# Performance work log

Measured on AMD Instinct MI355X. Metric: run time of the kernel, lower is better.

The kernel has to match this reference:

```python
import jax, jax.numpy as jnp
import numpy as np

N, L, S, C, H = 8, 1024, 1024, 256, 8
D = C // H  # 32

def setup_inputs() -> dict:
    key = jax.random.key(0)
    ks = jax.random.split(key, 9)
    sc = 1.0 / np.sqrt(C)
    return {
        "x": jax.random.normal(ks[0], (N, L, C), jnp.float32),
        "source1": jax.random.normal(ks[1], (N, S, C), jnp.float32),
        "x_embedding": jax.random.normal(ks[2], (N, L, C), jnp.float32),
        "source_embedding": jax.random.normal(ks[3], (N, S, C), jnp.float32),
        "Wq": jax.random.normal(ks[4], (C, C), jnp.float32) * sc,
        "Wk": jax.random.normal(ks[5], (C, C), jnp.float32) * sc,
        "Wv": jax.random.normal(ks[6], (C, C), jnp.float32) * sc,
        "Wp": jax.random.normal(ks[7], (C, C), jnp.float32) * sc,
        "bp": jnp.zeros((C,), jnp.float32),
    }

def reference(x, source1, x_embedding, source_embedding, Wq, Wk, Wv, Wp, bp):
    bs = x.shape[0]
    # torch `query += x_embedding` is IN-PLACE on x (same for source1),
    # so value projections also see embedding-added inputs.
    xq = x + x_embedding            # [N, L, C]
    sk = source1 + source_embedding  # [N, S, C]
    q = (xq @ Wq.T).reshape(bs, -1, H, D)   # [N, L, H, D]
    k = (sk @ Wk.T).reshape(bs, -1, H, D)   # [N, S, H, D]
    v1 = (xq @ Wv.T).reshape(bs, -1, H, D)  # [N, L, H, D]
    v2 = (sk @ Wv.T).reshape(bs, -1, H, D)  # [N, S, H, D]
    # Bilinear attention: softmax(q.k) aggregates v2, gated elementwise by v1.
    scores = jnp.einsum("nlhd,nshd->nlsh", q, k) / jnp.sqrt(jnp.float32(D))
    attn = jax.nn.softmax(scores, axis=2)          # softmax over source dim S
    message = v1 * jnp.einsum("nlsh,nshd->nlhd", attn, v2)  # [N, L, H, D]
    message = message.reshape(bs, -1, C)           # [N, L, C]
    return message @ Wp.T + bp
```

## Files before the change

### kernel.cpp

```cpp
#include <hip/hip_runtime.h>
#include <hip/hip_bf16.h>


typedef __bf16 bf16_t;
using bf16x8 = __attribute__((ext_vector_type(8))) __bf16;
using f32x4  = __attribute__((ext_vector_type(4))) float;

#define NB 8
#define LL 1024
#define SS 1024
#define CC 256
#define HH 8
#define DD 32
#define MTOK (NB * LL)

#define QSCALE (0.17677669529663688f * 1.4426950408889634f)

static __device__ __forceinline__ f32x4 mfma16(bf16x8 a, bf16x8 b, f32x4 c) {
  return __builtin_amdgcn_mfma_f32_16x16x32_bf16(a, b, c, 0, 0, 0);
}
static __device__ __forceinline__ float fexp2(float x) {
  return __builtin_amdgcn_exp2f(x);
}

__global__ __launch_bounds__(256) void wprep_kernel(
    const float* __restrict__ wq, const float* __restrict__ wk,
    const float* __restrict__ wv, const float* __restrict__ wp,
    bf16_t* __restrict__ Wall) {
  const int i = blockIdx.x * 256 + threadIdx.x;
  const int w = i >> 14, j = i & 16383;
  const float4* src = (const float4*)(w == 0 ? wq : w == 1 ? wk : w == 2 ? wv : wp);
  float4 v = src[j];
  bf16_t t4[4] __attribute__((aligned(8))) = {(bf16_t)v.x, (bf16_t)v.y,
                                              (bf16_t)v.z, (bf16_t)v.w};
  *(uint2*)(Wall + (size_t)w * CC * CC + 4 * (size_t)j) = *(const uint2*)t4;
}

__global__ __launch_bounds__(512) void proj_kernel(
    const float* __restrict__ x, const float* __restrict__ xe,
    const float* __restrict__ s1, const float* __restrict__ se,
    const bf16_t* __restrict__ Wall,
    bf16_t* __restrict__ Qw, bf16_t* __restrict__ Kw,
    bf16_t* __restrict__ V1w, bf16_t* __restrict__ V2T) {
  __shared__ __align__(16) bf16_t a_lds[64][264];

  const int tid = threadIdx.x;
  const int lane = tid & 63;
  const int wid = tid >> 6;
  const int r = lane & 15, g = lane >> 4;
  const int bm = blockIdx.x * 64;
  const int z = blockIdx.y;

  const float* A0 = z ? s1 : x;
  const float* A1 = z ? se : xe;
  const bf16_t* W0 = Wall + (size_t)z * CC * CC;
  const bf16_t* W1 = Wall + 2 * (size_t)CC * CC;

#pragma unroll
  for (int i = 0; i < 8; ++i) {
    const int f = i * 512 + tid;
    const int row = f >> 6, c4 = f & 63;
    float4 va = *(const float4*)(A0 + (size_t)(bm + row) * CC + c4 * 4);
    float4 vb = *(const float4*)(A1 + (size_t)(bm + row) * CC + c4 * 4);
    bf16_t t4[4] __attribute__((aligned(8))) = {
        (bf16_t)(va.x + vb.x), (bf16_t)(va.y + vb.y), (bf16_t)(va.z + vb.z),
        (bf16_t)(va.w + vb.w)};
    *(uint2*)&a_lds[row][c4 * 4] = *(const uint2*)t4;
  }
  __syncthreads();

  const int col_b0 = wid * 32;

  f32x4 acc0[4][2] = {};
  f32x4 acc1[4][2] = {};
#pragma unroll
  for (int k0 = 0; k0 < CC; k0 += 32) {
    bf16x8 a[4];
#pragma unroll
    for (int i = 0; i < 4; ++i)
      a[i] = *(const bf16x8*)&a_lds[i * 16 + r][k0 + g * 8];
    bf16x8 b00 = *(const bf16x8*)(W0 + (size_t)(col_b0 + r) * CC + k0 + g * 8);
    bf16x8 b01 = *(const bf16x8*)(W0 + (size_t)(col_b0 + 16 + r) * CC + k0 + g * 8);
    bf16x8 b10 = *(const bf16x8*)(W1 + (size_t)(col_b0 + r) * CC + k0 + g * 8);
    bf16x8 b11 = *(const bf16x8*)(W1 + (size_t)(col_b0 + 16 + r) * CC + k0 + g * 8);
#pragma unroll
    for (int i = 0; i < 4; ++i) {
      acc0[i][0] = mfma16(a[i], b00, acc0[i][0]);
      acc0[i][1] = mfma16(a[i], b01, acc0[i][1]);
      acc1[i][0] = mfma16(a[i], b10, acc1[i][0]);
      acc1[i][1] = mfma16(a[i], b11, acc1[i][1]);
    }
  }

#pragma unroll
  for (int i = 0; i < 4; ++i) {
#pragma unroll
    for (int j = 0; j < 2; ++j) {
      const int row_base = bm + i * 16 + g * 4;
      const int col = col_b0 + j * 16 + r;
      if (z == 0) {
#pragma unroll
        for (int t = 0; t < 4; ++t) {
          Qw[(size_t)(row_base + t) * CC + col] =
              (bf16_t)(acc0[i][j][t] * QSCALE);
          V1w[(size_t)(row_base + t) * CC + col] = (bf16_t)acc1[i][j][t];
        }
      } else {
#pragma unroll
        for (int t = 0; t < 4; ++t)
          Kw[(size_t)(row_base + t) * CC + col] = (bf16_t)acc0[i][j][t];
        const int n = row_base >> 10;
        const int s = row_base & (SS - 1);
        const int h = col >> 5;
        const int d = col & (DD - 1);
        bf16_t t4[4] __attribute__((aligned(8)));
#pragma unroll
        for (int t = 0; t < 4; ++t) t4[t] = (bf16_t)acc1[i][j][t];
        *(uint2*)(V2T + ((size_t)((n * HH + h) * DD + d)) * SS + s) =
            *(const uint2*)t4;
      }
    }
  }
}

__global__ __launch_bounds__(512) void attn_kernel(
    const bf16_t* __restrict__ Qw, const bf16_t* __restrict__ Kw,
    const bf16_t* __restrict__ V1w, const bf16_t* __restrict__ V2T,
    bf16_t* __restrict__ MSG) {
  __shared__ __align__(16) bf16_t k_lds[2][128][40];
  __shared__ __align__(16) bf16_t v_lds[2][32][136];

  const int tid = threadIdx.x;
  const int lane = tid & 63;
  const int wid = tid >> 6;
  const int r = lane & 15, g = lane >> 4;

  const int bid = blockIdx.x;
  const int work = (bid & 7) * 32 + (bid >> 3);
  const int grp = work >> 2;
  const int lt = work & 3;
  const int n = grp >> 3;
  const int h = grp & 7;
  const int l0 = lt * 256;
  const size_t tokQ = (size_t)n * LL + l0 + wid * 32;

  const bf16x8 qf0 = *(const bf16x8*)(Qw + (tokQ + r) * CC + h * DD + g * 8);
  const bf16x8 qf1 =
      *(const bf16x8*)(Qw + (tokQ + 16 + r) * CC + h * DD + g * 8);
  const bf16_t* Kb = Kw + ((size_t)n * SS) * CC + h * DD;
  const bf16_t* Vt = V2T + ((size_t)(n * HH + h)) * DD * SS;

  const int ktr = tid >> 2, ktq = tid & 3;
  const int kpr = (ktr & 96) | ((ktr & 4) << 2) | ((ktr & 24) >> 1) | (ktr & 3);
  const int vtr = tid >> 4, vtq = tid & 15;

  float lr0 = 0.f, lr1 = 0.f;
  const f32x4 zero = {0.f, 0.f, 0.f, 0.f};
  f32x4 o00 = zero, o01 = zero;
  f32x4 o10 = zero, o11 = zero;

  uint4 kra = *(const uint4*)(Kb + (size_t)ktr * CC + ktq * 8);
  uint4 vra = *(const uint4*)(Vt + (size_t)vtr * SS + vtq * 8);
  *(uint4*)&k_lds[0][kpr][ktq * 8] = kra;
  *(uint4*)&v_lds[0][vtr][vtq * 8] = vra;
  __syncthreads();

  for (int c = 0; c < 8; ++c) {
    const int cur = c & 1;
    if (c < 7) {
      const int s1 = (c + 1) * 128;
      kra = *(const uint4*)(Kb + (size_t)(s1 + ktr) * CC + ktq * 8);
      vra = *(const uint4*)(Vt + (size_t)vtr * SS + s1 + vtq * 8);
    }

    f32x4 pt0[8], pt1[8];
#pragma unroll
    for (int m = 0; m < 8; ++m) {
      bf16x8 kf = *(const bf16x8*)&k_lds[cur][m * 16 + r][g * 8];
      pt0[m] = mfma16(kf, qf0, zero);
      pt1[m] = mfma16(kf, qf1, zero);
    }

#pragma unroll
    for (int t = 0; t < 4; ++t) {
      float a0 = fexp2(pt0[2 * t][0]), a1 = fexp2(pt0[2 * t][1]);
      float a2 = fexp2(pt0[2 * t][2]), a3 = fexp2(pt0[2 * t][3]);
      float a4 = fexp2(pt0[2 * t + 1][0]), a5 = fexp2(pt0[2 * t + 1][1]);
      float a6 = fexp2(pt0[2 * t + 1][2]), a7 = fexp2(pt0[2 * t + 1][3]);
      float b0 = fexp2(pt1[2 * t][0]), b1 = fexp2(pt1[2 * t][1]);
      float b2 = fexp2(pt1[2 * t][2]), b3 = fexp2(pt1[2 * t][3]);
      float b4 = fexp2(pt1[2 * t + 1][0]), b5 = fexp2(pt1[2 * t + 1][1]);
      float b6 = fexp2(pt1[2 * t + 1][2]), b7 = fexp2(pt1[2 * t + 1][3]);
      lr0 += ((a0 + a1) + (a2 + a3)) + ((a4 + a5) + (a6 + a7));
      lr1 += ((b0 + b1) + (b2 + b3)) + ((b4 + b5) + (b6 + b7));
      bf16_t pa[8] __attribute__((aligned(16))) = {
          (bf16_t)a0, (bf16_t)a1, (bf16_t)a2, (bf16_t)a3,
          (bf16_t)a4, (bf16_t)a5, (bf16_t)a6, (bf16_t)a7};
      bf16_t pb[8] __attribute__((aligned(16))) = {
          (bf16_t)b0, (bf16_t)b1, (bf16_t)b2, (bf16_t)b3,
          (bf16_t)b4, (bf16_t)b5, (bf16_t)b6, (bf16_t)b7};
      bf16x8 pf0 = *(const bf16x8*)pa;
      bf16x8 pf1 = *(const bf16x8*)pb;
      bf16x8 va = *(const bf16x8*)&v_lds[cur][r][t * 32 + g * 8];
      bf16x8 vb = *(const bf16x8*)&v_lds[cur][16 + r][t * 32 + g * 8];
      o00 = mfma16(va, pf0, o00);
      o01 = mfma16(vb, pf0, o01);
      o10 = mfma16(va, pf1, o10);
      o11 = mfma16(vb, pf1, o11);
    }

    if (c < 7) {
      *(uint4*)&k_lds[cur ^ 1][kpr][ktq * 8] = kra;
      *(uint4*)&v_lds[cur ^ 1][vtr][vtq * 8] = vra;
    }
    __syncthreads();
  }

  lr0 += __shfl_xor(lr0, 16);
  lr0 += __shfl_xor(lr0, 32);
  lr1 += __shfl_xor(lr1, 16);
  lr1 += __shfl_xor(lr1, 32);
  const float li0 = 1.f / lr0, li1 = 1.f / lr1;

  const bf16_t* V1b0 = V1w + (tokQ + r) * CC + h * DD;
  const bf16_t* V1b1 = V1w + (tokQ + 16 + r) * CC + h * DD;
  bf16_t* Mb0 = MSG + (tokQ + r) * CC + h * DD;
  bf16_t* Mb1 = MSG + (tokQ + 16 + r) * CC + h * DD;
  uint2 u00 = *(const uint2*)(V1b0 + g * 4);
  uint2 u01 = *(const uint2*)(V1b0 + 16 + g * 4);
  uint2 u10 = *(const uint2*)(V1b1 + g * 4);
  uint2 u11 = *(const uint2*)(V1b1 + 16 + g * 4);
  const bf16_t* v00 = (const bf16_t*)&u00;
  const bf16_t* v01 = (const bf16_t*)&u01;
  const bf16_t* v10 = (const bf16_t*)&u10;
  const bf16_t* v11 = (const bf16_t*)&u11;
  bf16_t w00[4] __attribute__((aligned(8))), w01[4] __attribute__((aligned(8)));
  bf16_t w10[4] __attribute__((aligned(8))), w11[4] __attribute__((aligned(8)));
#pragma unroll
  for (int i = 0; i < 4; ++i) {
    w00[i] = (bf16_t)(o00[i] * li0 * (float)v00[i]);
    w01[i] = (bf16_t)(o01[i] * li0 * (float)v01[i]);
    w10[i] = (bf16_t)(o10[i] * li1 * (float)v10[i]);
    w11[i] = (bf16_t)(o11[i] * li1 * (float)v11[i]);
  }
  *(uint2*)(Mb0 + g * 4) = *(const uint2*)w00;
  *(uint2*)(Mb0 + 16 + g * 4) = *(const uint2*)w01;
  *(uint2*)(Mb1 + g * 4) = *(const uint2*)w10;
  *(uint2*)(Mb1 + 16 + g * 4) = *(const uint2*)w11;
}

__global__ __launch_bounds__(512) void out_kernel(
    const bf16_t* __restrict__ MSG, const bf16_t* __restrict__ Wp,
    const float* __restrict__ bp, float* __restrict__ out) {
  __shared__ __align__(16) bf16_t a_lds[32][264];

  const int tid = threadIdx.x;
  const int lane = tid & 63;
  const int wid = tid >> 6;
  const int r = lane & 15, g = lane >> 4;
  const int bm = blockIdx.x * 32;

#pragma unroll
  for (int i = 0; i < 2; ++i) {
    const int f = i * 512 + tid;
    const int row = f >> 5, c8 = f & 31;
    uint4 v = *(const uint4*)(MSG + (size_t)(bm + row) * CC + c8 * 8);
    *(uint4*)&a_lds[row][c8 * 8] = v;
  }
  __syncthreads();

  const int col_b0 = wid * 32;

  f32x4 acc[2][2] = {};
#pragma unroll
  for (int k0 = 0; k0 < CC; k0 += 32) {
    bf16x8 a[2];
#pragma unroll
    for (int i = 0; i < 2; ++i)
      a[i] = *(const bf16x8*)&a_lds[i * 16 + r][k0 + g * 8];
    bf16x8 b0 = *(const bf16x8*)(Wp + (size_t)(col_b0 + r) * CC + k0 + g * 8);
    bf16x8 b1 = *(const bf16x8*)(Wp + (size_t)(col_b0 + 16 + r) * CC + k0 + g * 8);
#pragma unroll
    for (int i = 0; i < 2; ++i) {
      acc[i][0] = mfma16(a[i], b0, acc[i][0]);
      acc[i][1] = mfma16(a[i], b1, acc[i][1]);
    }
  }

#pragma unroll
  for (int i = 0; i < 2; ++i) {
#pragma unroll
    for (int j = 0; j < 2; ++j) {
      const int row_base = bm + i * 16 + g * 4;
      const int col = col_b0 + j * 16 + r;
      const float bv = bp[col];
#pragma unroll
      for (int t = 0; t < 4; ++t)
        out[(size_t)(row_base + t) * CC + col] = acc[i][j][t] + bv;
    }
  }
}

extern "C" void kernel_launch(void* const* d_in, const int* in_sizes, int n_in,
                              void* d_out, int out_size, void* d_ws,
                              size_t ws_size, hipStream_t stream) {
  const float* x  = (const float*)d_in[0];
  const float* s1 = (const float*)d_in[1];
  const float* xe = (const float*)d_in[2];
  const float* se = (const float*)d_in[3];
  const float* Wq = (const float*)d_in[4];
  const float* Wk = (const float*)d_in[5];
  const float* Wv = (const float*)d_in[6];
  const float* Wp = (const float*)d_in[7];
  const float* bp = (const float*)d_in[8];
  float* out = (float*)d_out;

  char* ws = (char*)d_ws;
  bf16_t* Wall = (bf16_t*)(ws);
  bf16_t* Qw   = (bf16_t*)(ws + (1u << 20));
  bf16_t* Kw   = (bf16_t*)(ws + (5u << 20));
  bf16_t* V1w  = (bf16_t*)(ws + (9u << 20));
  bf16_t* V2T  = (bf16_t*)(ws + (13u << 20));
  bf16_t* MSG  = (bf16_t*)(ws + (17u << 20));
  bf16_t* Wpb  = Wall + 3 * CC * CC;

  wprep_kernel<<<256, 256, 0, stream>>>(Wq, Wk, Wv, Wp, Wall);
  proj_kernel<<<dim3(MTOK / 64, 2), 512, 0, stream>>>(
      x, xe, s1, se, Wall, Qw, Kw, V1w, V2T);
  attn_kernel<<<256, 512, 0, stream>>>(Qw, Kw, V1w, V2T, MSG);
  out_kernel<<<MTOK / 32, 512, 0, stream>>>(MSG, Wpb, bp, out);
}
```

Measured before the change: 49.31 us.

## Split projection A-tile load in halves and double attention chunk size

In the projection kernel, the A-tile conversion is split into two halves: the second half's fp32 loads are issued before the first half's MFMA loop and written to LDS afterward, so global loads overlap compute. In the attention kernel, the K/V chunk grows from 128 to 256 source positions, which halves the number of barriers and pipeline stages. The cost is higher LDS use (about double in attention) and more live registers, which may lower occupancy.

```diff
diff --git a/kernel.cpp b/kernel.cpp
--- a/kernel.cpp
+++ b/kernel.cpp
@@ -57,7 +57,7 @@
   const bf16_t* W1 = Wall + 2 * (size_t)CC * CC;
 
 #pragma unroll
-  for (int i = 0; i < 8; ++i) {
+  for (int i = 0; i < 4; ++i) {
     const int f = i * 512 + tid;
     const int row = f >> 6, c4 = f & 63;
     float4 va = *(const float4*)(A0 + (size_t)(bm + row) * CC + c4 * 4);
@@ -69,26 +69,66 @@
   }
   __syncthreads();
 
+  float4 va1[4], vb1[4];
+#pragma unroll
+  for (int i = 0; i < 4; ++i) {
+    const int f = 2048 + i * 512 + tid;
+    const int row = f >> 6, c4 = f & 63;
+    va1[i] = *(const float4*)(A0 + (size_t)(bm + row) * CC + c4 * 4);
+    vb1[i] = *(const float4*)(A1 + (size_t)(bm + row) * CC + c4 * 4);
+  }
+
   const int col_b0 = wid * 32;
 
   f32x4 acc0[4][2] = {};
   f32x4 acc1[4][2] = {};
+
 #pragma unroll
   for (int k0 = 0; k0 < CC; k0 += 32) {
-    bf16x8 a[4];
-#pragma unroll
-    for (int i = 0; i < 4; ++i)
+    bf16x8 a[2];
+#pragma unroll
+    for (int i = 0; i < 2; ++i)
       a[i] = *(const bf16x8*)&a_lds[i * 16 + r][k0 + g * 8];
     bf16x8 b00 = *(const bf16x8*)(W0 + (size_t)(col_b0 + r) * CC + k0 + g * 8);
     bf16x8 b01 = *(const bf16x8*)(W0 + (size_t)(col_b0 + 16 + r) * CC + k0 + g * 8);
     bf16x8 b10 = *(const bf16x8*)(W1 + (size_t)(col_b0 + r) * CC + k0 + g * 8);
     bf16x8 b11 = *(const bf16x8*)(W1 + (size_t)(col_b0 + 16 + r) * CC + k0 + g * 8);
 #pragma unroll
-    for (int i = 0; i < 4; ++i) {
+    for (int i = 0; i < 2; ++i) {
       acc0[i][0] = mfma16(a[i], b00, acc0[i][0]);
       acc0[i][1] = mfma16(a[i], b01, acc0[i][1]);
       acc1[i][0] = mfma16(a[i], b10, acc1[i][0]);
       acc1[i][1] = mfma16(a[i], b11, acc1[i][1]);
+    }
+  }
+
+#pragma unroll
+  for (int i = 0; i < 4; ++i) {
+    const int f = 2048 + i * 512 + tid;
+    const int row = f >> 6, c4 = f & 63;
+    bf16_t t4[4] __attribute__((aligned(8))) = {
+        (bf16_t)(va1[i].x + vb1[i].x), (bf16_t)(va1[i].y + vb1[i].y),
+        (bf16_t)(va1[i].z + vb1[i].z), (bf16_t)(va1[i].w + vb1[i].w)};
+    *(uint2*)&a_lds[row][c4 * 4] = *(const uint2*)t4;
+  }
+  __syncthreads();
+
+#pragma unroll
+  for (int k0 = 0; k0 < CC; k0 += 32) {
+    bf16x8 a[2];
+#pragma unroll
+    for (int i = 0; i < 2; ++i)
+      a[i] = *(const bf16x8*)&a_lds[32 + i * 16 + r][k0 + g * 8];
+    bf16x8 b00 = *(const bf16x8*)(W0 + (size_t)(col_b0 + r) * CC + k0 + g * 8);
+    bf16x8 b01 = *(const bf16x8*)(W0 + (size_t)(col_b0 + 16 + r) * CC + k0 + g * 8);
+    bf16x8 b10 = *(const bf16x8*)(W1 + (size_t)(col_b0 + r) * CC + k0 + g * 8);
+    bf16x8 b11 = *(const bf16x8*)(W1 + (size_t)(col_b0 + 16 + r) * CC + k0 + g * 8);
+#pragma unroll
+    for (int i = 0; i < 2; ++i) {
+      acc0[2 + i][0] = mfma16(a[i], b00, acc0[2 + i][0]);
+      acc0[2 + i][1] = mfma16(a[i], b01, acc0[2 + i][1]);
+      acc1[2 + i][0] = mfma16(a[i], b10, acc1[2 + i][0]);
+      acc1[2 + i][1] = mfma16(a[i], b11, acc1[2 + i][1]);
     }
   }
 
@@ -127,8 +167,8 @@
     const bf16_t* __restrict__ Qw, const bf16_t* __restrict__ Kw,
     const bf16_t* __restrict__ V1w, const bf16_t* __restrict__ V2T,
     bf16_t* __restrict__ MSG) {
-  __shared__ __align__(16) bf16_t k_lds[2][128][40];
-  __shared__ __align__(16) bf16_t v_lds[2][32][136];
+  __shared__ __align__(16) bf16_t k_lds[2][256][40];
+  __shared__ __align__(16) bf16_t v_lds[2][32][264];
 
   const int tid = threadIdx.x;
   const int lane = tid & 63;
@@ -160,58 +200,71 @@
   f32x4 o10 = zero, o11 = zero;
 
   uint4 kra = *(const uint4*)(Kb + (size_t)ktr * CC + ktq * 8);
+  uint4 krb = *(const uint4*)(Kb + (size_t)(128 + ktr) * CC + ktq * 8);
   uint4 vra = *(const uint4*)(Vt + (size_t)vtr * SS + vtq * 8);
+  uint4 vrb = *(const uint4*)(Vt + (size_t)vtr * SS + 128 + vtq * 8);
   *(uint4*)&k_lds[0][kpr][ktq * 8] = kra;
+  *(uint4*)&k_lds[0][128 + kpr][ktq * 8] = krb;
   *(uint4*)&v_lds[0][vtr][vtq * 8] = vra;
+  *(uint4*)&v_lds[0][vtr][128 + vtq * 8] = vrb;
   __syncthreads();
 
-  for (int c = 0; c < 8; ++c) {
+  for (int c = 0; c < 4; ++c) {
     const int cur = c & 1;
-    if (c < 7) {
-      const int s1 = (c + 1) * 128;
+    if (c < 3) {
+      const int s1 = (c + 1) * 256;
       kra = *(const uint4*)(Kb + (size_t)(s1 + ktr) * CC + ktq * 8);
+      krb = *(const uint4*)(Kb + (size_t)(s1 + 128 + ktr) * CC + ktq * 8);
       vra = *(const uint4*)(Vt + (size_t)vtr * SS + s1 + vtq * 8);
-    }
-
-    f32x4 pt0[8], pt1[8];
-#pragma unroll
-    for (int m = 0; m < 8; ++m) {
-      bf16x8 kf = *(const bf16x8*)&k_lds[cur][m * 16 + r][g * 8];
-      pt0[m] = mfma16(kf, qf0, zero);
-      pt1[m] = mfma16(kf, qf1, zero);
-    }
-
-#pragma unroll
-    for (int t = 0; t < 4; ++t) {
-      float a0 = fexp2(pt0[2 * t][0]), a1 = fexp2(pt0[2 * t][1]);
-      float a2 = fexp2(pt0[2 * t][2]), a3 = fexp2(pt0[2 * t][3]);
-      float a4 = fexp2(pt0[2 * t + 1][0]), a5 = fexp2(pt0[2 * t + 1][1]);
-      float a6 = fexp2(pt0[2 * t + 1][2]), a7 = fexp2(pt0[2 * t + 1][3]);
-      float b0 = fexp2(pt1[2 * t][0]), b1 = fexp2(pt1[2 * t][1]);
-      float b2 = fexp2(pt1[2 * t][2]), b3 = fexp2(pt1[2 * t][3]);
-      float b4 = fexp2(pt1[2 * t + 1][0]), b5 = fexp2(pt1[2 * t + 1][1]);
-      float b6 = fexp2(pt1[2 * t + 1][2]), b7 = fexp2(pt1[2 * t + 1][3]);
-      lr0 += ((a0 + a1) + (a2 + a3)) + ((a4 + a5) + (a6 + a7));
-      lr1 += ((b0 + b1) + (b2 + b3)) + ((b4 + b5) + (b6 + b7));
-      bf16_t pa[8] __attribute__((aligned(16))) = {
-          (bf16_t)a0, (bf16_t)a1, (bf16_t)a2, (bf16_t)a3,
-          (bf16_t)a4, (bf16_t)a5, (bf16_t)a6, (bf16_t)a7};
-      bf16_t pb[8] __attribute__((aligned(16))) = {
-          (bf16_t)b0, (bf16_t)b1, (bf16_t)b2, (bf16_t)b3,
-          (bf16_t)b4, (bf16_t)b5, (bf16_t)b6, (bf16_t)b7};
-      bf16x8 pf0 = *(const bf16x8*)pa;
-      bf16x8 pf1 = *(const bf16x8*)pb;
-      bf16x8 va = *(const bf16x8*)&v_lds[cur][r][t * 32 + g * 8];
-      bf16x8 vb = *(const bf16x8*)&v_lds[cur][16 + r][t * 32 + g * 8];
-      o00 = mfma16(va, pf0, o00);
-      o01 = mfma16(vb, pf0, o01);
-      o10 = mfma16(va, pf1, o10);
-      o11 = mfma16(vb, pf1, o11);
-    }
-
-    if (c < 7) {
+      vrb = *(const uint4*)(Vt + (size_t)vtr * SS + s1 + 128 + vtq * 8);
+    }
+
+#pragma unroll
+    for (int hh = 0; hh < 2; ++hh) {
+      f32x4 pt0[8], pt1[8];
+#pragma unroll
+      for (int m = 0; m < 8; ++m) {
+        bf16x8 kf = *(const bf16x8*)&k_lds[cur][hh * 128 + m * 16 + r][g * 8];
+        pt0[m] = mfma16(kf, qf0, zero);
+        pt1[m] = mfma16(kf, qf1, zero);
+      }
+
+#pragma unroll
+      for (int t = 0; t < 4; ++t) {
+        float a0 = fexp2(pt0[2 * t][0]), a1 = fexp2(pt0[2 * t][1]);
+        float a2 = fexp2(pt0[2 * t][2]), a3 = fexp2(pt0[2 * t][3]);
+        float a4 = fexp2(pt0[2 * t + 1][0]), a5 = fexp2(pt0[2 * t + 1][1]);
+        float a6 = fexp2(pt0[2 * t + 1][2]), a7 = fexp2(pt0[2 * t + 1][3]);
+        float b0 = fexp2(pt1[2 * t][0]), b1 = fexp2(pt1[2 * t][1]);
+        float b2 = fexp2(pt1[2 * t][2]), b3 = fexp2(pt1[2 * t][3]);
+        float b4 = fexp2(pt1[2 * t + 1][0]), b5 = fexp2(pt1[2 * t + 1][1]);
+        float b6 = fexp2(pt1[2 * t + 1][2]), b7 = fexp2(pt1[2 * t + 1][3]);
+        lr0 += ((a0 + a1) + (a2 + a3)) + ((a4 + a5) + (a6 + a7));
+        lr1 += ((b0 + b1) + (b2 + b3)) + ((b4 + b5) + (b6 + b7));
+        bf16_t pa[8] __attribute__((aligned(16))) = {
+            (bf16_t)a0, (bf16_t)a1, (bf16_t)a2, (bf16_t)a3,
+            (bf16_t)a4, (bf16_t)a5, (bf16_t)a6, (bf16_t)a7};
+        bf16_t pb[8] __attribute__((aligned(16))) = {
+            (bf16_t)b0, (bf16_t)b1, (bf16_t)b2, (bf16_t)b3,
+            (bf16_t)b4, (bf16_t)b5, (bf16_t)b6, (bf16_t)b7};
+        bf16x8 pf0 = *(const bf16x8*)pa;
+        bf16x8 pf1 = *(const bf16x8*)pb;
+        bf16x8 va =
+            *(const bf16x8*)&v_lds[cur][r][hh * 128 + t * 32 + g * 8];
+        bf16x8 vb =
+            *(const bf16x8*)&v_lds[cur][16 + r][hh * 128 + t * 32 + g * 8];
+        o00 = mfma16(va, pf0, o00);
+        o01 = mfma16(vb, pf0, o01);
+        o10 = mfma16(va, pf1, o10);
+        o11 = mfma16(vb, pf1, o11);
+      }
+    }
+
+    if (c < 3) {
       *(uint4*)&k_lds[cur ^ 1][kpr][ktq * 8] = kra;
+      *(uint4*)&k_lds[cur ^ 1][128 + kpr][ktq * 8] = krb;
       *(uint4*)&v_lds[cur ^ 1][vtr][vtq * 8] = vra;
+      *(uint4*)&v_lds[cur ^ 1][vtr][128 + vtq * 8] = vrb;
     }
     __syncthreads();
   }
```

Result: slower. 54.59 us (+10.7%).
